# Performance work log

Measured on AMD Instinct MI355X. Metric: run time of the kernel, lower is better.

Reference implementation:

```python
import jax, jax.numpy as jnp
import numpy as np

D_MODEL = 1024
D_STATE = 16
D_CONV = 4
EXPAND = 2
D_INNER = EXPAND * D_MODEL
DT_RANK = (D_MODEL + 15) // 16  # ceil(d_model/16) = 64


def setup_inputs() -> dict:
    key = jax.random.key(0)
    ks = jax.random.split(key, 12)
    B, L = 2, 2048
    s = lambda k, shape, sc: jax.random.normal(k, shape, dtype=jnp.float32) * sc
    inp = {
        "x": s(ks[0], (B, L, D_MODEL), 1.0),
        "in_proj_w": s(ks[1], (2 * D_INNER, D_MODEL), 0.02),
        "conv_w": s(ks[2], (D_INNER, 1, D_CONV), 0.2),
        "conv_b": s(ks[3], (D_INNER,), 0.02),
        "x_proj_w": s(ks[4], (DT_RANK + 2 * D_STATE, D_INNER), 0.02),
        "dt_proj_w": s(ks[5], (D_INNER, DT_RANK), 0.05),
        "dt_proj_b": s(ks[6], (D_INNER,), 0.5),
        # A_log init: log(1..d_state) per channel (standard S4D-real init)
        "A_log": jnp.broadcast_to(jnp.log(jnp.arange(1, D_STATE + 1, dtype=jnp.float32)), (D_INNER, D_STATE)).copy(),
        "D": jnp.ones((D_INNER,), dtype=jnp.float32),
        "out_proj_w": s(ks[7], (D_MODEL, D_INNER), 0.02),
        "ln_g": jnp.ones((D_MODEL,), dtype=jnp.float32),
        "ln_b": jnp.zeros((D_MODEL,), dtype=jnp.float32),
    }
    return inp


def _mamba(x, in_proj_w, conv_w, conv_b, x_proj_w, dt_proj_w, dt_proj_b, A_log, D, out_proj_w):
    Bsz, L, _ = x.shape
    # input projection -> x branch and gate z
    xz = jnp.einsum("bld,ed->ble", x, in_proj_w)  # [B, L, 2*d_inner]
    xi, z = jnp.split(xz, 2, axis=-1)
    # causal depthwise conv over time
    xc = jnp.swapaxes(xi, 1, 2)  # [B, d_inner, L]
    xc = jax.lax.conv_general_dilated(
        xc, conv_w, window_strides=(1,), padding=[(D_CONV - 1, 0)],
        feature_group_count=D_INNER, dimension_numbers=("NCH", "OIH", "NCH"))
    xc = xc + conv_b[None, :, None]
    xc = jnp.swapaxes(xc, 1, 2)  # [B, L, d_inner]
    xc = jax.nn.silu(xc)
    # data-dependent dt, B, C
    x_dbl = jnp.einsum("bld,ed->ble", xc, x_proj_w)
    dt_r = x_dbl[..., :DT_RANK]
    Bm = x_dbl[..., DT_RANK:DT_RANK + D_STATE]      # [B, L, d_state]
    Cm = x_dbl[..., DT_RANK + D_STATE:]             # [B, L, d_state]
    dt = jax.nn.softplus(jnp.einsum("blr,er->ble", dt_r, dt_proj_w) + dt_proj_b)  # [B, L, d_inner]
    A = -jnp.exp(A_log)  # [d_inner, d_state]

    # selective scan: h_t = exp(dt_t*A) h_{t-1} + dt_t*B_t*u_t ; y_t = C_t . h_t
    def step(h, inps):
        dt_t, B_t, C_t, u_t = inps  # [B,d_inner],[B,d_state],[B,d_state],[B,d_inner]
        dA = jnp.exp(dt_t[..., None] * A)                       # [B, d_inner, d_state]
        dBu = (dt_t * u_t)[..., None] * B_t[:, None, :]          # [B, d_inner, d_state]
        h = dA * h + dBu
        y = jnp.einsum("bds,bs->bd", h, C_t)
        return h, y

    h0 = jnp.zeros((Bsz, D_INNER, D_STATE), dtype=x.dtype)
    xs = (jnp.swapaxes(dt, 0, 1), jnp.swapaxes(Bm, 0, 1), jnp.swapaxes(Cm, 0, 1), jnp.swapaxes(xc, 0, 1))
    _, ys = jax.lax.scan(step, h0, xs)
    y = jnp.swapaxes(ys, 0, 1) + D * xc  # skip term
    y = y * jax.nn.silu(z)
    return jnp.einsum("ble,de->bld", y, out_proj_w)


def _layernorm(x, g, b, eps=1e-5):
    mu = jnp.mean(x, axis=-1, keepdims=True)
    var = jnp.mean(jnp.square(x - mu), axis=-1, keepdims=True)
    return (x - mu) * jax.lax.rsqrt(var + eps) * g + b


def reference(x, in_proj_w, conv_w, conv_b, x_proj_w, dt_proj_w, dt_proj_b, A_log, D, out_proj_w, ln_g, ln_b):
    y = _mamba(x, in_proj_w, conv_w, conv_b, x_proj_w, dt_proj_w, dt_proj_b, A_log, D, out_proj_w)
    return _layernorm(y + x, ln_g, ln_b)
```

## Files before the change

### kernel.cpp

```cpp
#include <hip/hip_runtime.h>
#include <math.h>

#define D_STATE 16
#define D_INNER 2048
#define SEQ     2048
#define BSZ     2
#define NTOK    (BSZ*SEQ)
#define CH      32
#define NCHK    (SEQ/CH)
#define PHN     ((size_t)BSZ * NCHK * 2048 * 16)

typedef __bf16 bf16x8 __attribute__((ext_vector_type(8)));
typedef float  floatx4 __attribute__((ext_vector_type(4)));

__device__ __forceinline__ unsigned short f2bf(float f) {
  unsigned int u = __float_as_uint(f);
  u += 0x7fff + ((u >> 16) & 1);
  return (unsigned short)(u >> 16);
}
__device__ __forceinline__ float bf2f(unsigned short u) {
  return __uint_as_float((unsigned int)u << 16);
}

__device__ __forceinline__ void gload16(const unsigned short* g, unsigned short* l) {
  __builtin_amdgcn_global_load_lds(
      (const __attribute__((address_space(1))) unsigned int*)g,
      (__attribute__((address_space(3))) unsigned int*)l, 16, 0, 0);
}

__global__ __launch_bounds__(256) void cast_k(
    const float* __restrict__ src, unsigned short* __restrict__ dst, int n)
{
  int i = (blockIdx.x * 256 + threadIdx.x) * 4;
  if (i < n) {
    float4 v = *(const float4*)(src + i);
    ushort4 o;
    o.x = f2bf(v.x); o.y = f2bf(v.y); o.z = f2bf(v.z); o.w = f2bf(v.w);
    *(ushort4*)(dst + i) = o;
  }
}

__global__ __launch_bounds__(256) void cast2_k(
    const float* __restrict__ s1, unsigned short* __restrict__ d1, int n1,
    const float* __restrict__ s2, unsigned short* __restrict__ d2, int n2)
{
  int i = (blockIdx.x * 256 + threadIdx.x) * 4;
  const float* s; unsigned short* d;
  if (i < n1) { s = s1 + i; d = d1 + i; }
  else if (i < n1 + n2) { s = s2 + (i - n1); d = d2 + (i - n1); }
  else return;
  float4 v = *(const float4*)s;
  ushort4 o;
  o.x = f2bf(v.x); o.y = f2bf(v.y); o.z = f2bf(v.z); o.w = f2bf(v.w);
  *(ushort4*)d = o;
}

__global__ __launch_bounds__(256) void redcast_k(
    const float* __restrict__ p, float* __restrict__ dst,
    unsigned short* __restrict__ dtr)
{
  int i = (blockIdx.x * 256 + threadIdx.x) * 4;
  float4 s = *(const float4*)(p + i);
#pragma unroll
  for (int z = 1; z < 8; ++z) {
    float4 v = *(const float4*)(p + (size_t)z * (4096 * 96) + i);
    s.x += v.x; s.y += v.y; s.z += v.z; s.w += v.w;
  }
  *(float4*)(dst + i) = s;
  int m = i / 96, col = i - m * 96;
  if (col < 64) {
    ushort4 o;
    o.x = f2bf(s.x); o.y = f2bf(s.y); o.z = f2bf(s.z); o.w = f2bf(s.w);
    *(ushort4*)(dtr + (size_t)m * 64 + col) = o;
  }
}

template<int MODE>
__global__ __launch_bounds__(256) void mgemm(
    const unsigned short* __restrict__ A, int lda,
    const unsigned short* __restrict__ W, int ldw,
    void* __restrict__ Cv_, int ldc,
    int N, int ksl, const float* __restrict__ aux, size_t slicesz)
{
  __shared__ unsigned short As[128 * 32];
  __shared__ unsigned short Ws[128 * 32];
  const int tid  = threadIdx.x;
  const int wave = tid >> 6, lane = tid & 63;
  const int m0 = blockIdx.y * 128, n0 = blockIdx.x * 128;
  const int k0 = blockIdx.z * ksl;
  const int srow = lane >> 2;
  const int scol = ((((lane & 3) + 4) - ((lane >> 3) & 3)) & 3) * 8;
  const int fr = lane & 15, fq = lane >> 4;
  const int sw = (fr >> 1) & 3;
  const int wm = (wave >> 1) * 64, wn = (wave & 1) * 64;

  const int ar0 = (wave * 2 + 0) * 16 + srow;
  const int ar1 = (wave * 2 + 1) * 16 + srow;
  int wr0 = n0 + ar0; if (wr0 > N - 1) wr0 = N - 1;
  int wr1 = n0 + ar1; if (wr1 > N - 1) wr1 = N - 1;
  const unsigned short* gA0 = A + (size_t)(m0 + ar0) * lda + scol;
  const unsigned short* gA1 = A + (size_t)(m0 + ar1) * lda + scol;
  const unsigned short* gW0 = W + (size_t)wr0 * ldw + scol;
  const unsigned short* gW1 = W + (size_t)wr1 * ldw + scol;
  unsigned short* lA0 = As + (wave * 2 + 0) * 512;
  unsigned short* lA1 = As + (wave * 2 + 1) * 512;
  unsigned short* lW0 = Ws + (wave * 2 + 0) * 512;
  unsigned short* lW1 = Ws + (wave * 2 + 1) * 512;

  floatx4 zero = {0.f, 0.f, 0.f, 0.f};
  floatx4 acc[4][4];
#pragma unroll
  for (int i = 0; i < 4; ++i)
#pragma unroll
    for (int j = 0; j < 4; ++j) acc[i][j] = zero;

  for (int kt = k0; kt < k0 + ksl; kt += 32) {
    __syncthreads();
    gload16(gA0 + kt, lA0);
    gload16(gA1 + kt, lA1);
    gload16(gW0 + kt, lW0);
    gload16(gW1 + kt, lW1);
    __syncthreads();
    bf16x8 af[4], bfr[4];
#pragma unroll
    for (int i = 0; i < 4; ++i) {
      int cuA = ((fq + sw) & 3) * 8;
      af[i]  = *(const bf16x8*)(As + (wm + i * 16 + fr) * 32 + cuA);
      bfr[i] = *(const bf16x8*)(Ws + (wn + i * 16 + fr) * 32 + cuA);
    }
#pragma unroll
    for (int i = 0; i < 4; ++i)
#pragma unroll
      for (int j = 0; j < 4; ++j)
        acc[i][j] = __builtin_amdgcn_mfma_f32_16x16x32_bf16(af[i], bfr[j], acc[i][j], 0, 0, 0);
  }

#pragma unroll
  for (int i = 0; i < 4; ++i) {
#pragma unroll
    for (int j = 0; j < 4; ++j) {
      int n = n0 + wn + j * 16 + fr;
      if (n < N) {
#pragma unroll
        for (int r = 0; r < 4; ++r) {
          int m = m0 + wm + i * 16 + fq * 4 + r;
          float v = acc[i][j][r];
          if (MODE == 1) { v += aux[n]; v = (v > 20.f) ? v : log1pf(__expf(v)); }
          if (MODE == 3) {
            ((unsigned short*)Cv_)[(size_t)m * ldc + n] = f2bf(v);
          } else {
            float* C = (float*)Cv_ + (size_t)blockIdx.z * slicesz;
            C[(size_t)m * ldc + n] = v;
          }
        }
      }
    }
  }
}

__global__ __launch_bounds__(256) void conv_silu_k(
    const unsigned short* __restrict__ xzb, const float* __restrict__ w,
    const float* __restrict__ b, unsigned short* __restrict__ xcb)
{
  int gid = blockIdx.x * 256 + threadIdx.x;
  int e4 = (gid * 4) & 2047;
  int bl = gid >> 9;
  int l  = bl & (SEQ - 1);
  float4 acc = *(const float4*)(b + e4);
  float4 w0 = *(const float4*)(w + (e4 + 0) * 4);
  float4 w1 = *(const float4*)(w + (e4 + 1) * 4);
  float4 w2 = *(const float4*)(w + (e4 + 2) * 4);
  float4 w3 = *(const float4*)(w + (e4 + 3) * 4);
  const float* w0p = (const float*)&w0;
  const float* w1p = (const float*)&w1;
  const float* w2p = (const float*)&w2;
  const float* w3p = (const float*)&w3;
#pragma unroll
  for (int k = 0; k < 4; ++k) {
    int ll = l - 3 + k;
    if (ll >= 0) {
      ushort4 xv = *(const ushort4*)(xzb + (size_t)(bl - 3 + k) * 4096 + e4);
      acc.x = fmaf(bf2f(xv.x), w0p[k], acc.x);
      acc.y = fmaf(bf2f(xv.y), w1p[k], acc.y);
      acc.z = fmaf(bf2f(xv.z), w2p[k], acc.z);
      acc.w = fmaf(bf2f(xv.w), w3p[k], acc.w);
    }
  }
  ushort4 o;
  o.x = f2bf(acc.x / (1.f + __expf(-acc.x)));
  o.y = f2bf(acc.y / (1.f + __expf(-acc.y)));
  o.z = f2bf(acc.z / (1.f + __expf(-acc.z)));
  o.w = f2bf(acc.w / (1.f + __expf(-acc.w)));
  *(ushort4*)(xcb + (size_t)gid * 4) = o;
}

__global__ __launch_bounds__(256) void scan_p1(
    const float* __restrict__ A_log,
    const float* __restrict__ x_dbl, const unsigned short* __restrict__ xcb,
    const float* __restrict__ dt, float* __restrict__ PH)
{
  const int t = blockIdx.x * 256 + threadIdx.x;
  const int d = t & 2047;
  const int c = (t >> 11) & (NCHK - 1);
  const int b = t >> 17;
  const size_t tok0 = (size_t)b * SEQ + c * CH;
  const float* xd = x_dbl + tok0 * 96;

  float Ac[16];
  {
    float4 a0 = *(const float4*)(A_log + d * 16);
    float4 a1 = *(const float4*)(A_log + d * 16 + 4);
    float4 a2 = *(const float4*)(A_log + d * 16 + 8);
    float4 a3 = *(const float4*)(A_log + d * 16 + 12);
    Ac[0]=-__expf(a0.x); Ac[1]=-__expf(a0.y); Ac[2]=-__expf(a0.z); Ac[3]=-__expf(a0.w);
    Ac[4]=-__expf(a1.x); Ac[5]=-__expf(a1.y); Ac[6]=-__expf(a1.z); Ac[7]=-__expf(a1.w);
    Ac[8]=-__expf(a2.x); Ac[9]=-__expf(a2.y); Ac[10]=-__expf(a2.z); Ac[11]=-__expf(a2.w);
    Ac[12]=-__expf(a3.x); Ac[13]=-__expf(a3.y); Ac[14]=-__expf(a3.z); Ac[15]=-__expf(a3.w);
  }

  float p[16], h[16];
#pragma unroll
  for (int s = 0; s < 16; ++s) { p[s] = 1.f; h[s] = 0.f; }

  for (int l = 0; l < CH; ++l) {
    float dtv = dt[(tok0 + l) * 2048 + d];
    float uv  = bf2f(xcb[(tok0 + l) * 2048 + d]);
    float du  = dtv * uv;
    float Bv[16];
#pragma unroll
    for (int j = 0; j < 4; ++j) {
      float4 bb = *(const float4*)(xd + l * 96 + 64 + j * 4);
      Bv[j*4+0]=bb.x; Bv[j*4+1]=bb.y; Bv[j*4+2]=bb.z; Bv[j*4+3]=bb.w;
    }
#pragma unroll
    for (int s = 0; s < 16; ++s) {
      float dA = __expf(dtv * Ac[s]);
      p[s] *= dA;
      h[s] = fmaf(dA, h[s], du * Bv[s]);
    }
  }

  float* pp = PH + (size_t)t * 16;
#pragma unroll
  for (int j = 0; j < 4; ++j) {
    *(float4*)(pp + j * 4)       = make_float4(p[j*4], p[j*4+1], p[j*4+2], p[j*4+3]);
    *(float4*)(pp + PHN + j * 4) = make_float4(h[j*4], h[j*4+1], h[j*4+2], h[j*4+3]);
  }
}

__global__ __launch_bounds__(256) void scan_fix(float* __restrict__ PH)
{
  int tid = blockIdx.x * 256 + threadIdx.x;
  int s = tid & 15;
  int d = (tid >> 4) & 2047;
  int b = tid >> 15;
  float h = 0.f;
  for (int c = 0; c < NCHK; ++c) {
    size_t idx = ((((size_t)(b * NCHK + c) * 2048) + d) * 16) + s;
    float p  = PH[idx];
    float hl = PH[idx + PHN];
    PH[idx + PHN] = h;
    h = fmaf(p, h, hl);
  }
}

__global__ __launch_bounds__(256) void scan_p2(
    const float* __restrict__ A_log, const float* __restrict__ Dvec,
    const float* __restrict__ x_dbl, const unsigned short* __restrict__ xcb,
    const unsigned short* __restrict__ xzb, const float* __restrict__ PH,
    const float* __restrict__ dt, unsigned short* __restrict__ ybf)
{
  const int t = blockIdx.x * 256 + threadIdx.x;
  const int d = t & 2047;
  const int c = (t >> 11) & (NCHK - 1);
  const int b = t >> 17;
  const size_t tok0 = (size_t)b * SEQ + c * CH;
  const float* xd = x_dbl + tok0 * 96;
  const float Dd = Dvec[d];

  float Ac[16];
  {
    float4 a0 = *(const float4*)(A_log + d * 16);
    float4 a1 = *(const float4*)(A_log + d * 16 + 4);
    float4 a2 = *(const float4*)(A_log + d * 16 + 8);
    float4 a3 = *(const float4*)(A_log + d * 16 + 12);
    Ac[0]=-__expf(a0.x); Ac[1]=-__expf(a0.y); Ac[2]=-__expf(a0.z); Ac[3]=-__expf(a0.w);
    Ac[4]=-__expf(a1.x); Ac[5]=-__expf(a1.y); Ac[6]=-__expf(a1.z); Ac[7]=-__expf(a1.w);
    Ac[8]=-__expf(a2.x); Ac[9]=-__expf(a2.y); Ac[10]=-__expf(a2.z); Ac[11]=-__expf(a2.w);
    Ac[12]=-__expf(a3.x); Ac[13]=-__expf(a3.y); Ac[14]=-__expf(a3.z); Ac[15]=-__expf(a3.w);
  }

  const float* pp = PH + (size_t)t * 16;
  float h[16];
#pragma unroll
  for (int j = 0; j < 4; ++j) {
    float4 hh = *(const float4*)(pp + PHN + j * 4);
    h[j*4+0]=hh.x; h[j*4+1]=hh.y; h[j*4+2]=hh.z; h[j*4+3]=hh.w;
  }

  for (int l = 0; l < CH; ++l) {
    float dtv = dt[(tok0 + l) * 2048 + d];
    float uv  = bf2f(xcb[(tok0 + l) * 2048 + d]);
    float zv  = bf2f(xzb[(tok0 + l) * 4096 + 2048 + d]);
    float du  = dtv * uv;
    float Bv[16], Cv[16];
#pragma unroll
    for (int j = 0; j < 4; ++j) {
      float4 bb = *(const float4*)(xd + l * 96 + 64 + j * 4);
      float4 cc = *(const float4*)(xd + l * 96 + 80 + j * 4);
      Bv[j*4+0]=bb.x; Bv[j*4+1]=bb.y; Bv[j*4+2]=bb.z; Bv[j*4+3]=bb.w;
      Cv[j*4+0]=cc.x; Cv[j*4+1]=cc.y; Cv[j*4+2]=cc.z; Cv[j*4+3]=cc.w;
    }
    float y = 0.f;
#pragma unroll
    for (int s = 0; s < 16; ++s) {
      float dA = __expf(dtv * Ac[s]);
      h[s] = fmaf(dA, h[s], du * Bv[s]);
      y = fmaf(h[s], Cv[s], y);
    }
    y = fmaf(Dd, uv, y);
    y *= zv / (1.f + __expf(-zv));
    ybf[(tok0 + l) * 2048 + d] = f2bf(y);
  }
}

__global__ __launch_bounds__(256) void ln2_k(
    const float* __restrict__ p0, const float* __restrict__ p1,
    const float* __restrict__ x, const float* __restrict__ g,
    const float* __restrict__ bb, float* __restrict__ out)
{
  int row = blockIdx.x;
  size_t off = (size_t)row * 1024;
  float4 a = ((const float4*)(p0 + off))[threadIdx.x];
  float4 b = ((const float4*)(p1 + off))[threadIdx.x];
  float4 c = ((const float4*)(x  + off))[threadIdx.x];
  float4 v;
  v.x = a.x + b.x + c.x; v.y = a.y + b.y + c.y;
  v.z = a.z + b.z + c.z; v.w = a.w + b.w + c.w;
  float s  = v.x + v.y + v.z + v.w;
  float sq = v.x * v.x + v.y * v.y + v.z * v.z + v.w * v.w;
#pragma unroll
  for (int o = 32; o >= 1; o >>= 1) {
    s  += __shfl_xor(s,  o, 64);
    sq += __shfl_xor(sq, o, 64);
  }
  __shared__ float red[8];
  int wid = threadIdx.x >> 6;
  if ((threadIdx.x & 63) == 0) { red[wid] = s; red[4 + wid] = sq; }
  __syncthreads();
  s  = red[0] + red[1] + red[2] + red[3];
  sq = red[4] + red[5] + red[6] + red[7];
  float mu  = s * (1.f / 1024.f);
  float var = sq * (1.f / 1024.f) - mu * mu;
  float r   = rsqrtf(var + 1e-5f);
  int col = threadIdx.x * 4;
  float4 gv = *(const float4*)(g + col);
  float4 bv = *(const float4*)(bb + col);
  float4 o;
  o.x = (v.x - mu) * r * gv.x + bv.x;
  o.y = (v.y - mu) * r * gv.y + bv.y;
  o.z = (v.z - mu) * r * gv.z + bv.z;
  o.w = (v.w - mu) * r * gv.w + bv.w;
  ((float4*)(out + off))[threadIdx.x] = o;
}

extern "C" void kernel_launch(void* const* d_in, const int* in_sizes, int n_in,
                              void* d_out, int out_size, void* d_ws, size_t ws_size,
                              hipStream_t stream)
{
  const float* x       = (const float*)d_in[0];
  const float* in_proj = (const float*)d_in[1];
  const float* conv_w  = (const float*)d_in[2];
  const float* conv_b  = (const float*)d_in[3];
  const float* x_proj  = (const float*)d_in[4];
  const float* dt_w    = (const float*)d_in[5];
  const float* dt_b    = (const float*)d_in[6];
  const float* A_log   = (const float*)d_in[7];
  const float* Dv      = (const float*)d_in[8];
  const float* out_w   = (const float*)d_in[9];
  const float* ln_g    = (const float*)d_in[10];
  const float* ln_bias = (const float*)d_in[11];
  float* out = (float*)d_out;

  char* w8 = (char*)d_ws;
  unsigned short* xz_bf = (unsigned short*)w8;
  unsigned short* xc_bf = (unsigned short*)(w8 + 33554432);
  float*          xdbl  = (float*)(w8 + 50331648);
  float*          dty   = (float*)(w8 + 51904512);
  unsigned short* y_bf  = (unsigned short*)(w8 + 85458944);
  unsigned short* wbuf  = (unsigned short*)(w8 + 102236160);
  unsigned short* x_bf  = (unsigned short*)(w8 + 110624768);
  float*          pbufx = (float*)(w8 + 119013376);
  float*          PH    = (float*)(w8 + 131596288);
  float*          pbufo = (float*)xz_bf;

  dim3 blk(256);
  cast2_k<<<dim3(2 * NTOK * 1024 / 1024), blk, 0, stream>>>(
      x, x_bf, NTOK * 1024, in_proj, wbuf, 4096 * 1024);
  mgemm<3><<<dim3(32, 32, 1), blk, 0, stream>>>(x_bf, 1024, wbuf, 1024,
                                                xz_bf, 4096, 4096, 1024, nullptr, 0);
  conv_silu_k<<<dim3((NTOK * D_INNER / 4) / 256), blk, 0, stream>>>(
      xz_bf, conv_w, conv_b, xc_bf);
  cast_k<<<dim3(96 * 2048 / 1024), blk, 0, stream>>>(x_proj, wbuf, 96 * 2048);
  mgemm<0><<<dim3(1, 32, 8), blk, 0, stream>>>(xc_bf, 2048, wbuf, 2048,
                                               pbufx, 96, 96, 256, nullptr,
                                               (size_t)4096 * 96);
  redcast_k<<<dim3(4096 * 96 / 1024), blk, 0, stream>>>(pbufx, xdbl, x_bf );
  cast_k<<<dim3(2048 * 64 / 1024), blk, 0, stream>>>(dt_w, wbuf, 2048 * 64);
  mgemm<1><<<dim3(16, 32, 1), blk, 0, stream>>>(x_bf , 64, wbuf, 64,
                                                dty, 2048, 2048, 64, dt_b, 0);
  scan_p1 <<<dim3(BSZ * NCHK * 2048 / 256), blk, 0, stream>>>(A_log, xdbl, xc_bf, dty, PH);
  scan_fix<<<dim3(BSZ * 2048 * 16 / 256), blk, 0, stream>>>(PH);
  scan_p2 <<<dim3(BSZ * NCHK * 2048 / 256), blk, 0, stream>>>(A_log, Dv, xdbl, xc_bf,
                                                              xz_bf, PH, dty, y_bf);
  cast_k<<<dim3(1024 * 2048 / 1024), blk, 0, stream>>>(out_w, wbuf, 1024 * 2048);
  mgemm<0><<<dim3(8, 32, 2), blk, 0, stream>>>(y_bf, 2048, wbuf, 2048,
                                               pbufo, 1024, 1024, 1024, nullptr,
                                               (size_t)4096 * 1024);
  ln2_k<<<dim3(NTOK), blk, 0, stream>>>(pbufo, pbufo + (size_t)4096 * 1024,
                                        x, ln_g, ln_bias, out);
}
```

Baseline: 379.1 us.

## Fuse weight casts into one kernel, unroll GEMM k-loop, store dt as bf16

```diff
diff --git a/kernel.cpp b/kernel.cpp
--- a/kernel.cpp
+++ b/kernel.cpp
@@ -28,26 +28,27 @@
       (__attribute__((address_space(3))) unsigned int*)l, 16, 0, 0);
 }
 
-__global__ __launch_bounds__(256) void cast_k(
-    const float* __restrict__ src, unsigned short* __restrict__ dst, int n)
-{
-  int i = (blockIdx.x * 256 + threadIdx.x) * 4;
-  if (i < n) {
-    float4 v = *(const float4*)(src + i);
-    ushort4 o;
-    o.x = f2bf(v.x); o.y = f2bf(v.y); o.z = f2bf(v.z); o.w = f2bf(v.w);
-    *(ushort4*)(dst + i) = o;
-  }
-}
-
-__global__ __launch_bounds__(256) void cast2_k(
-    const float* __restrict__ s1, unsigned short* __restrict__ d1, int n1,
-    const float* __restrict__ s2, unsigned short* __restrict__ d2, int n2)
+#define N_X   (NTOK*1024)
+#define N_WI  (4096*1024)
+#define N_WX  (96*2048)
+#define N_WD  (2048*64)
+#define N_WO  (1024*2048)
+#define N_ALL (N_X+N_WI+N_WX+N_WD+N_WO)
+
+__global__ __launch_bounds__(256) void cast5_k(
+    const float* __restrict__ sx, unsigned short* __restrict__ dx,
+    const float* __restrict__ swi, unsigned short* __restrict__ dwi,
+    const float* __restrict__ swx, unsigned short* __restrict__ dwx,
+    const float* __restrict__ swd, unsigned short* __restrict__ dwd,
+    const float* __restrict__ swo, unsigned short* __restrict__ dwo)
 {
   int i = (blockIdx.x * 256 + threadIdx.x) * 4;
   const float* s; unsigned short* d;
-  if (i < n1) { s = s1 + i; d = d1 + i; }
-  else if (i < n1 + n2) { s = s2 + (i - n1); d = d2 + (i - n1); }
+  if      (i < N_X)                  { s = sx  + i;                      d = dx  + i; }
+  else if (i < N_X+N_WI)             { s = swi + (i - N_X);              d = dwi + (i - N_X); }
+  else if (i < N_X+N_WI+N_WX)        { s = swx + (i - N_X-N_WI);         d = dwx + (i - N_X-N_WI); }
+  else if (i < N_X+N_WI+N_WX+N_WD)   { s = swd + (i - N_X-N_WI-N_WX);    d = dwd + (i - N_X-N_WI-N_WX); }
+  else if (i < N_ALL)                { s = swo + (i - N_X-N_WI-N_WX-N_WD); d = dwo + (i - N_X-N_WI-N_WX-N_WD); }
   else return;
   float4 v = *(const float4*)s;
   ushort4 o;
@@ -82,8 +83,8 @@
     void* __restrict__ Cv_, int ldc,
     int N, int ksl, const float* __restrict__ aux, size_t slicesz)
 {
-  __shared__ unsigned short As[128 * 32];
-  __shared__ unsigned short Ws[128 * 32];
+  __shared__ unsigned short As[2][128 * 32];
+  __shared__ unsigned short Ws[2][128 * 32];
   const int tid  = threadIdx.x;
   const int wave = tid >> 6, lane = tid & 63;
   const int m0 = blockIdx.y * 128, n0 = blockIdx.x * 128;
@@ -102,10 +103,8 @@
   const unsigned short* gA1 = A + (size_t)(m0 + ar1) * lda + scol;
   const unsigned short* gW0 = W + (size_t)wr0 * ldw + scol;
   const unsigned short* gW1 = W + (size_t)wr1 * ldw + scol;
-  unsigned short* lA0 = As + (wave * 2 + 0) * 512;
-  unsigned short* lA1 = As + (wave * 2 + 1) * 512;
-  unsigned short* lW0 = Ws + (wave * 2 + 0) * 512;
-  unsigned short* lW1 = Ws + (wave * 2 + 1) * 512;
+  const int lofs0 = (wave * 2 + 0) * 512;
+  const int lofs1 = (wave * 2 + 1) * 512;
 
   floatx4 zero = {0.f, 0.f, 0.f, 0.f};
   floatx4 acc[4][4];
@@ -114,25 +113,32 @@
 #pragma unroll
     for (int j = 0; j < 4; ++j) acc[i][j] = zero;
 
-  for (int kt = k0; kt < k0 + ksl; kt += 32) {
+  for (int kt = k0; kt < k0 + ksl; kt += 64) {
     __syncthreads();
-    gload16(gA0 + kt, lA0);
-    gload16(gA1 + kt, lA1);
-    gload16(gW0 + kt, lW0);
-    gload16(gW1 + kt, lW1);
+    gload16(gA0 + kt,      As[0] + lofs0);
+    gload16(gA1 + kt,      As[0] + lofs1);
+    gload16(gW0 + kt,      Ws[0] + lofs0);
+    gload16(gW1 + kt,      Ws[0] + lofs1);
+    gload16(gA0 + kt + 32, As[1] + lofs0);
+    gload16(gA1 + kt + 32, As[1] + lofs1);
+    gload16(gW0 + kt + 32, Ws[1] + lofs0);
+    gload16(gW1 + kt + 32, Ws[1] + lofs1);
     __syncthreads();
-    bf16x8 af[4], bfr[4];
-#pragma unroll
-    for (int i = 0; i < 4; ++i) {
-      int cuA = ((fq + sw) & 3) * 8;
-      af[i]  = *(const bf16x8*)(As + (wm + i * 16 + fr) * 32 + cuA);
-      bfr[i] = *(const bf16x8*)(Ws + (wn + i * 16 + fr) * 32 + cuA);
-    }
-#pragma unroll
-    for (int i = 0; i < 4; ++i)
-#pragma unroll
-      for (int j = 0; j < 4; ++j)
-        acc[i][j] = __builtin_amdgcn_mfma_f32_16x16x32_bf16(af[i], bfr[j], acc[i][j], 0, 0, 0);
+#pragma unroll
+    for (int kb = 0; kb < 2; ++kb) {
+      bf16x8 af[4], bfr[4];
+      const int cuA = ((fq + sw) & 3) * 8;
+#pragma unroll
+      for (int i = 0; i < 4; ++i) {
+        af[i]  = *(const bf16x8*)(As[kb] + (wm + i * 16 + fr) * 32 + cuA);
+        bfr[i] = *(const bf16x8*)(Ws[kb] + (wn + i * 16 + fr) * 32 + cuA);
+      }
+#pragma unroll
+      for (int i = 0; i < 4; ++i)
+#pragma unroll
+        for (int j = 0; j < 4; ++j)
+          acc[i][j] = __builtin_amdgcn_mfma_f32_16x16x32_bf16(af[i], bfr[j], acc[i][j], 0, 0, 0);
+    }
   }
 
 #pragma unroll
@@ -145,8 +151,10 @@
         for (int r = 0; r < 4; ++r) {
           int m = m0 + wm + i * 16 + fq * 4 + r;
           float v = acc[i][j][r];
-          if (MODE == 1) { v += aux[n]; v = (v > 20.f) ? v : log1pf(__expf(v)); }
-          if (MODE == 3) {
+          if (MODE == 1) {
+            v += aux[n]; v = (v > 20.f) ? v : log1pf(__expf(v));
+            ((unsigned short*)Cv_)[(size_t)m * ldc + n] = f2bf(v);
+          } else if (MODE == 3) {
             ((unsigned short*)Cv_)[(size_t)m * ldc + n] = f2bf(v);
           } else {
             float* C = (float*)Cv_ + (size_t)blockIdx.z * slicesz;
@@ -197,7 +205,7 @@
 __global__ __launch_bounds__(256) void scan_p1(
     const float* __restrict__ A_log,
     const float* __restrict__ x_dbl, const unsigned short* __restrict__ xcb,
-    const float* __restrict__ dt, float* __restrict__ PH)
+    const unsigned short* __restrict__ dtb, float* __restrict__ PH)
 {
   const int t = blockIdx.x * 256 + threadIdx.x;
   const int d = t & 2047;
@@ -223,7 +231,7 @@
   for (int s = 0; s < 16; ++s) { p[s] = 1.f; h[s] = 0.f; }
 
   for (int l = 0; l < CH; ++l) {
-    float dtv = dt[(tok0 + l) * 2048 + d];
+    float dtv = bf2f(dtb[(tok0 + l) * 2048 + d]);
     float uv  = bf2f(xcb[(tok0 + l) * 2048 + d]);
     float du  = dtv * uv;
     float Bv[16];
@@ -268,7 +276,7 @@
     const float* __restrict__ A_log, const float* __restrict__ Dvec,
     const float* __restrict__ x_dbl, const unsigned short* __restrict__ xcb,
     const unsigned short* __restrict__ xzb, const float* __restrict__ PH,
-    const float* __restrict__ dt, unsigned short* __restrict__ ybf)
+    const unsigned short* __restrict__ dtb, unsigned short* __restrict__ ybf)
 {
   const int t = blockIdx.x * 256 + threadIdx.x;
   const int d = t & 2047;
@@ -299,7 +307,7 @@
   }
 
   for (int l = 0; l < CH; ++l) {
-    float dtv = dt[(tok0 + l) * 2048 + d];
+    float dtv = bf2f(dtb[(tok0 + l) * 2048 + d]);
     float uv  = bf2f(xcb[(tok0 + l) * 2048 + d]);
     float zv  = bf2f(xzb[(tok0 + l) * 4096 + 2048 + d]);
     float du  = dtv * uv;
@@ -383,38 +391,38 @@
   float* out = (float*)d_out;
 
   char* w8 = (char*)d_ws;
-  unsigned short* xz_bf = (unsigned short*)w8;
+  unsigned short* xz_bf = (unsigned short*)(w8 + 0);
   unsigned short* xc_bf = (unsigned short*)(w8 + 33554432);
   float*          xdbl  = (float*)(w8 + 50331648);
-  float*          dty   = (float*)(w8 + 51904512);
-  unsigned short* y_bf  = (unsigned short*)(w8 + 85458944);
-  unsigned short* wbuf  = (unsigned short*)(w8 + 102236160);
-  unsigned short* x_bf  = (unsigned short*)(w8 + 110624768);
-  float*          pbufx = (float*)(w8 + 119013376);
-  float*          PH    = (float*)(w8 + 131596288);
+  unsigned short* dty   = (unsigned short*)(w8 + 51904512);
+  unsigned short* y_bf  = (unsigned short*)(w8 + 68681728);
+  unsigned short* x_bf  = (unsigned short*)(w8 + 85458944);
+  unsigned short* w_in  = (unsigned short*)(w8 + 93847552);
+  unsigned short* w_x   = (unsigned short*)(w8 + 102236160);
+  unsigned short* w_dt  = (unsigned short*)(w8 + 102629376);
+  unsigned short* w_out = (unsigned short*)(w8 + 102891520);
+  float*          pbufx = (float*)(w8 + 107085824);
+  float*          PH    = (float*)(w8 + 119668736);
   float*          pbufo = (float*)xz_bf;
 
   dim3 blk(256);
-  cast2_k<<<dim3(2 * NTOK * 1024 / 1024), blk, 0, stream>>>(
-      x, x_bf, NTOK * 1024, in_proj, wbuf, 4096 * 1024);
-  mgemm<3><<<dim3(32, 32, 1), blk, 0, stream>>>(x_bf, 1024, wbuf, 1024,
+  cast5_k<<<dim3((N_ALL / 4 + 255) / 256), blk, 0, stream>>>(
+      x, x_bf, in_proj, w_in, x_proj, w_x, dt_w, w_dt, out_w, w_out);
+  mgemm<3><<<dim3(32, 32, 1), blk, 0, stream>>>(x_bf, 1024, w_in, 1024,
                                                 xz_bf, 4096, 4096, 1024, nullptr, 0);
   conv_silu_k<<<dim3((NTOK * D_INNER / 4) / 256), blk, 0, stream>>>(
       xz_bf, conv_w, conv_b, xc_bf);
-  cast_k<<<dim3(96 * 2048 / 1024), blk, 0, stream>>>(x_proj, wbuf, 96 * 2048);
-  mgemm<0><<<dim3(1, 32, 8), blk, 0, stream>>>(xc_bf, 2048, wbuf, 2048,
+  mgemm<0><<<dim3(1, 32, 8), blk, 0, stream>>>(xc_bf, 2048, w_x, 2048,
                                                pbufx, 96, 96, 256, nullptr,
                                                (size_t)4096 * 96);
   redcast_k<<<dim3(4096 * 96 / 1024), blk, 0, stream>>>(pbufx, xdbl, x_bf );
-  cast_k<<<dim3(2048 * 64 / 1024), blk, 0, stream>>>(dt_w, wbuf, 2048 * 64);
-  mgemm<1><<<dim3(16, 32, 1), blk, 0, stream>>>(x_bf , 64, wbuf, 64,
+  mgemm<1><<<dim3(16, 32, 1), blk, 0, stream>>>(x_bf , 64, w_dt, 64,
                                                 dty, 2048, 2048, 64, dt_b, 0);
   scan_p1 <<<dim3(BSZ * NCHK * 2048 / 256), blk, 0, stream>>>(A_log, xdbl, xc_bf, dty, PH);
   scan_fix<<<dim3(BSZ * 2048 * 16 / 256), blk, 0, stream>>>(PH);
   scan_p2 <<<dim3(BSZ * NCHK * 2048 / 256), blk, 0, stream>>>(A_log, Dv, xdbl, xc_bf,
                                                               xz_bf, PH, dty, y_bf);
-  cast_k<<<dim3(1024 * 2048 / 1024), blk, 0, stream>>>(out_w, wbuf, 1024 * 2048);
-  mgemm<0><<<dim3(8, 32, 2), blk, 0, stream>>>(y_bf, 2048, wbuf, 2048,
+  mgemm<0><<<dim3(8, 32, 2), blk, 0, stream>>>(y_bf, 2048, w_out, 2048,
                                                pbufo, 1024, 1024, 1024, nullptr,
                                                (size_t)4096 * 1024);
   ln2_k<<<dim3(NTOK), blk, 0, stream>>>(pbufo, pbufo + (size_t)4096 * 1024,
```

New measurement: 362.5 us. 1.05x faster.
